# Optimization experiments

Hardware: AMD Instinct MI355X
Metric: run time of the kernel (lower is better)

Reference implementation:

```python
import jax, jax.numpy as jnp
import numpy as np

T = 0.07          # temperature (params[1])
B, N, D, C = 128, 100000, 128, 40  # batch, bank size (outputSize=K), feat dim (inputSize-1), n classes
STDV = 1.0 / np.sqrt((D + 1) / 3.0)  # init scale from __init__


def setup_inputs() -> dict:
    key = jax.random.key(0)
    k1, k2, k3, k4, k5, k6 = jax.random.split(key, 6)
    x = jax.random.normal(k1, (B, D), dtype=jnp.float32)
    x = x / jnp.linalg.norm(x, axis=1, keepdims=True)  # unit-norm features (keeps exp(out/T) in range)
    y = jax.random.randint(k2, (B,), 0, N)
    labels = jax.random.randint(k3, (B,), 0, C)
    bank_labels = jax.random.randint(k4, (N,), 0, C).astype(jnp.float32)
    mem_feats = (jax.random.uniform(k5, (N, D), dtype=jnp.float32) * 2.0 - 1.0) * STDV
    da_feats = (jax.random.uniform(k6, (N, D), dtype=jnp.float32) * 2.0 - 1.0) * STDV
    memory = jnp.concatenate([bank_labels[:, None], mem_feats], axis=1)      # [N, 1+D], col 0 = label
    memory_da = jnp.concatenate([bank_labels[:, None], da_feats], axis=1)    # [N, 1+D], col 0 = label
    return {"x": x, "y": y, "labels": labels, "memory_da": memory_da, "memory": memory}


def reference(x, y, labels, memory_da, memory):
    # NCEFunction.forward: out[b,n] = exp(x[b] . memory_da[n,1:] / T), Z-normalized per row (Z<0 branch)
    n_out = memory_da.shape[0]
    feats = memory_da[:, 1:]                               # [N, D] gathered features
    out = jnp.exp(jnp.einsum('bd,nd->bn', x, feats) / T)   # [B, N] (torch bmm over repeated bank)
    Z1 = out.mean(axis=1, keepdims=True) * n_out           # per-row Z estimate
    out = out / Z1
    # idx: per-label torch.where loop -> expressed densely as a boolean match matrix [B, N]
    idx_mask = memory_da[None, :, 0] == labels[:, None].astype(memory_da.dtype)
    return out, idx_mask
```

## Files before the change

kernel.cpp:

```cpp
#include <hip/hip_runtime.h>
#include <hip/hip_bf16.h>

#define NB 128
#define NMEM 100000
#define ND 128
constexpr float T_INV = 1.0f / 0.07f;

constexpr int LROW = ND + 8;
constexpr int TILE = 128;
constexpr int NTILES = (NMEM + TILE - 1) / TILE;
constexpr int ZSTRIDE = 16;
constexpr int C4FULL = TILE * 129 / 4;
constexpr int NITER = (C4FULL + 255) / 256;

typedef __attribute__((ext_vector_type(8))) __bf16 bf16x8;
typedef __attribute__((ext_vector_type(4))) float f32x4;
struct bf4 { __bf16 a, b, c, d; };

template<bool PASS2>
__global__ __launch_bounds__(256, 2) void nce_pass(
    const float* __restrict__ x,
    const int* __restrict__ labels,
    const float* __restrict__ mem_da,
    float* __restrict__ zbuf,
    float* __restrict__ out,
    float* __restrict__ maskout)
{
  __shared__ __bf16 xs[NB * LROW];
  __shared__ __bf16 fs[TILE * LROW];
  __shared__ float lbl_n[TILE];
  __shared__ float lbl_b[NB];
  __shared__ float rz[NB];
  __shared__ float zl[NB];

  const int tid = threadIdx.x;
  const int t = blockIdx.x;
  const int count4 = (t == NTILES - 1) ? (NMEM - t * TILE) * 129 / 4 : C4FULL;

  const float4* f4 = (const float4*)(mem_da + (size_t)t * (TILE * 129));
  float4 fv[NITER];
  #pragma unroll
  for (int i = 0; i < NITER; ++i) {
    int idx = tid + i * 256;
    fv[i] = f4[idx < count4 ? idx : 0];
  }
  const float4* x4 = (const float4*)x;
  float4 xv[16];
  #pragma unroll
  for (int i = 0; i < 16; ++i) xv[i] = x4[tid + i * 256];

  #pragma unroll
  for (int i = 0; i < 16; ++i) {
    int g4 = tid + i * 256;
    int row = g4 >> 5;
    int col = (g4 & 31) * 4;
    *(bf4*)&xs[row * LROW + col] =
        bf4{(__bf16)xv[i].x, (__bf16)xv[i].y, (__bf16)xv[i].z, (__bf16)xv[i].w};
  }

  #pragma unroll
  for (int i = 0; i < NITER; ++i) {
    int idx = tid + i * 256;
    if (idx < count4) {
      unsigned g = 4u * (unsigned)idx;
      unsigned r = g / 129u;
      unsigned cc = g - r * 129u;
      float4 v = fv[i];
      #pragma unroll
      for (int c = 0; c < 4; ++c) {
        float val = (&v.x)[c];
        if (cc == 0) lbl_n[r] = val;
        else fs[r * LROW + (cc - 1)] = (__bf16)val;
        if (++cc == 129u) { cc = 0; ++r; }
      }
    }
  }

  if (tid < NB) {
    lbl_b[tid] = (float)labels[tid];
    if (PASS2) rz[tid] = 1.0f / zbuf[tid * ZSTRIDE];
    else zl[tid] = 0.0f;
  }
  __syncthreads();

  const int wid = tid >> 6;
  const int lane = tid & 63;
  const int q = lane >> 4;
  const int l16 = lane & 15;
  const int nbase = t * TILE + wid * 32;

  if (nbase < NMEM) {
    f32x4 acc[8][2];
    #pragma unroll
    for (int mt = 0; mt < 8; ++mt) {
      acc[mt][0] = (f32x4){0.f, 0.f, 0.f, 0.f};
      acc[mt][1] = (f32x4){0.f, 0.f, 0.f, 0.f};
    }
    #pragma unroll
    for (int kc = 0; kc < 4; ++kc) {
      const int ko = kc * 32 + q * 8;
      bf16x8 b0 = *(const bf16x8*)&fs[(wid * 32 + l16) * LROW + ko];
      bf16x8 b1 = *(const bf16x8*)&fs[(wid * 32 + 16 + l16) * LROW + ko];
      #pragma unroll
      for (int mt = 0; mt < 8; ++mt) {
        bf16x8 a = *(const bf16x8*)&xs[(mt * 16 + l16) * LROW + ko];
        acc[mt][0] = __builtin_amdgcn_mfma_f32_16x16x32_bf16(a, b0, acc[mt][0], 0, 0, 0);
        acc[mt][1] = __builtin_amdgcn_mfma_f32_16x16x32_bf16(a, b1, acc[mt][1], 0, 0, 0);
      }
    }

    if (!PASS2) {
      float ln0 = lbl_n[wid * 32 + l16];
      float ln1 = lbl_n[wid * 32 + 16 + l16];
      #pragma unroll
      for (int mt = 0; mt < 8; ++mt) {
        #pragma unroll
        for (int r = 0; r < 4; ++r) {
          int m = mt * 16 + q * 4 + r;
          float lb = lbl_b[m];
          size_t base = (size_t)m * NMEM + nbase + l16;
          maskout[base]      = (ln0 == lb) ? 1.0f : 0.0f;
          maskout[base + 16] = (ln1 == lb) ? 1.0f : 0.0f;
          float v = __expf(acc[mt][0][r] * T_INV) + __expf(acc[mt][1][r] * T_INV);
          v += __shfl_xor(v, 1);
          v += __shfl_xor(v, 2);
          v += __shfl_xor(v, 4);
          v += __shfl_xor(v, 8);
          if (l16 == 0) atomicAdd(&zl[m], v);
        }
      }
    } else {
      #pragma unroll
      for (int mt = 0; mt < 8; ++mt) {
        #pragma unroll
        for (int r = 0; r < 4; ++r) {
          int m = mt * 16 + q * 4 + r;
          float rzm = rz[m];
          size_t base = (size_t)m * NMEM + nbase + l16;
          out[base]      = __expf(acc[mt][0][r] * T_INV) * rzm;
          out[base + 16] = __expf(acc[mt][1][r] * T_INV) * rzm;
        }
      }
    }
  }

  if (!PASS2) {
    __syncthreads();
    if (tid < NB) atomicAdd(&zbuf[tid * ZSTRIDE], zl[tid]);
  }
}

extern "C" void kernel_launch(void* const* d_in, const int* in_sizes, int n_in,
                              void* d_out, int out_size, void* d_ws, size_t ws_size,
                              hipStream_t stream) {
  const float* x      = (const float*)d_in[0];
  const int* labels   = (const int*)d_in[2];
  const float* mem_da = (const float*)d_in[3];
  float* out     = (float*)d_out;
  float* maskout = out + (size_t)NB * NMEM;
  float* zbuf    = (float*)d_ws;

  hipMemsetAsync(zbuf, 0, NB * ZSTRIDE * sizeof(float), stream);
  nce_pass<false><<<NTILES, 256, 0, stream>>>(x, labels, mem_da, zbuf, nullptr, maskout);
  nce_pass<true ><<<NTILES, 256, 0, stream>>>(x, labels, mem_da, zbuf, out, nullptr);
}
```

Before: 224.9 us.

## Convert both passes to persistent blocks with atomic tile queue and register prefetch

Replaces the one-block-per-tile launch with a fixed 512-block persistent grid that pulls tiles from a global atomic counter. While the current tile is computed, each block prefetches the next tile's memory bank rows into registers. This spreads the x staging and per-block setup over many tiles and overlaps global loads with MFMA and store work. The cost is an extra atomic and a barrier per tile, plus higher register pressure from holding the prefetch buffer alongside the accumulators.

```diff
diff --git a/kernel.cpp b/kernel.cpp
--- a/kernel.cpp
+++ b/kernel.cpp
@@ -8,10 +8,11 @@
 
 constexpr int LROW = ND + 8;
 constexpr int TILE = 128;
-constexpr int NTILES = (NMEM + TILE - 1) / TILE;
+constexpr int NT = (NMEM + TILE - 1) / TILE;
+constexpr int C4FULL = TILE * 129 / 4;
+constexpr int NIT = 17;
 constexpr int ZSTRIDE = 16;
-constexpr int C4FULL = TILE * 129 / 4;
-constexpr int NITER = (C4FULL + 255) / 256;
+constexpr int GRID = 512;
 
 typedef __attribute__((ext_vector_type(8))) __bf16 bf16x8;
 typedef __attribute__((ext_vector_type(4))) float f32x4;
@@ -23,6 +24,7 @@
     const int* __restrict__ labels,
     const float* __restrict__ mem_da,
     float* __restrict__ zbuf,
+    int* __restrict__ ctr,
     float* __restrict__ out,
     float* __restrict__ maskout)
 {
@@ -32,120 +34,129 @@
   __shared__ float lbl_b[NB];
   __shared__ float rz[NB];
   __shared__ float zl[NB];
+  __shared__ int cur;
 
   const int tid = threadIdx.x;
-  const int t = blockIdx.x;
-  const int count4 = (t == NTILES - 1) ? (NMEM - t * TILE) * 129 / 4 : C4FULL;
 
-  const float4* f4 = (const float4*)(mem_da + (size_t)t * (TILE * 129));
-  float4 fv[NITER];
-  #pragma unroll
-  for (int i = 0; i < NITER; ++i) {
-    int idx = tid + i * 256;
-    fv[i] = f4[idx < count4 ? idx : 0];
-  }
   const float4* x4 = (const float4*)x;
   float4 xv[16];
   #pragma unroll
   for (int i = 0; i < 16; ++i) xv[i] = x4[tid + i * 256];
-
   #pragma unroll
   for (int i = 0; i < 16; ++i) {
     int g4 = tid + i * 256;
-    int row = g4 >> 5;
-    int col = (g4 & 31) * 4;
-    *(bf4*)&xs[row * LROW + col] =
+    *(bf4*)&xs[(g4 >> 5) * LROW + (g4 & 31) * 4] =
         bf4{(__bf16)xv[i].x, (__bf16)xv[i].y, (__bf16)xv[i].z, (__bf16)xv[i].w};
   }
-
-  #pragma unroll
-  for (int i = 0; i < NITER; ++i) {
-    int idx = tid + i * 256;
-    if (idx < count4) {
-      unsigned g = 4u * (unsigned)idx;
-      unsigned r = g / 129u;
-      unsigned cc = g - r * 129u;
-      float4 v = fv[i];
-      #pragma unroll
-      for (int c = 0; c < 4; ++c) {
-        float val = (&v.x)[c];
-        if (cc == 0) lbl_n[r] = val;
-        else fs[r * LROW + (cc - 1)] = (__bf16)val;
-        if (++cc == 129u) { cc = 0; ++r; }
-      }
-    }
-  }
-
   if (tid < NB) {
     lbl_b[tid] = (float)labels[tid];
     if (PASS2) rz[tid] = 1.0f / zbuf[tid * ZSTRIDE];
-    else zl[tid] = 0.0f;
+    else zl[tid] = 0.f;
   }
+
+  if (tid == 0) cur = atomicAdd(ctr, 1);
   __syncthreads();
+  int t = cur;
 
-  const int wid = tid >> 6;
-  const int lane = tid & 63;
-  const int q = lane >> 4;
-  const int l16 = lane & 15;
-  const int nbase = t * TILE + wid * 32;
+  float4 fv[NIT];
+  auto prefetch = [&](int tt) {
+    const float4* f4 = (const float4*)(mem_da + (size_t)tt * (TILE * 129));
+    const int c4 = (tt == NT - 1) ? (NMEM - tt * TILE) * 129 / 4 : C4FULL;
+    #pragma unroll
+    for (int i = 0; i < NIT; ++i) {
+      int idx = tid + i * 256;
+      fv[i] = f4[idx < c4 ? idx : 0];
+    }
+  };
+  if (t < NT) prefetch(t);
 
-  if (nbase < NMEM) {
-    f32x4 acc[8][2];
+  const int wid = tid >> 6, lane = tid & 63, q = lane >> 4, l16 = lane & 15;
+
+  while (t < NT) {
+    const int rows = min(TILE, NMEM - t * TILE);
+    const int c4 = rows * 129 / 4;
     #pragma unroll
-    for (int mt = 0; mt < 8; ++mt) {
-      acc[mt][0] = (f32x4){0.f, 0.f, 0.f, 0.f};
-      acc[mt][1] = (f32x4){0.f, 0.f, 0.f, 0.f};
-    }
-    #pragma unroll
-    for (int kc = 0; kc < 4; ++kc) {
-      const int ko = kc * 32 + q * 8;
-      bf16x8 b0 = *(const bf16x8*)&fs[(wid * 32 + l16) * LROW + ko];
-      bf16x8 b1 = *(const bf16x8*)&fs[(wid * 32 + 16 + l16) * LROW + ko];
-      #pragma unroll
-      for (int mt = 0; mt < 8; ++mt) {
-        bf16x8 a = *(const bf16x8*)&xs[(mt * 16 + l16) * LROW + ko];
-        acc[mt][0] = __builtin_amdgcn_mfma_f32_16x16x32_bf16(a, b0, acc[mt][0], 0, 0, 0);
-        acc[mt][1] = __builtin_amdgcn_mfma_f32_16x16x32_bf16(a, b1, acc[mt][1], 0, 0, 0);
-      }
-    }
-
-    if (!PASS2) {
-      float ln0 = lbl_n[wid * 32 + l16];
-      float ln1 = lbl_n[wid * 32 + 16 + l16];
-      #pragma unroll
-      for (int mt = 0; mt < 8; ++mt) {
+    for (int i = 0; i < NIT; ++i) {
+      int idx = tid + i * 256;
+      if (idx < c4) {
+        unsigned g = 4u * (unsigned)idx;
+        unsigned r = g / 129u;
+        unsigned cc = g - r * 129u;
+        float4 v = fv[i];
         #pragma unroll
-        for (int r = 0; r < 4; ++r) {
-          int m = mt * 16 + q * 4 + r;
-          float lb = lbl_b[m];
-          size_t base = (size_t)m * NMEM + nbase + l16;
-          maskout[base]      = (ln0 == lb) ? 1.0f : 0.0f;
-          maskout[base + 16] = (ln1 == lb) ? 1.0f : 0.0f;
-          float v = __expf(acc[mt][0][r] * T_INV) + __expf(acc[mt][1][r] * T_INV);
-          v += __shfl_xor(v, 1);
-          v += __shfl_xor(v, 2);
-          v += __shfl_xor(v, 4);
-          v += __shfl_xor(v, 8);
-          if (l16 == 0) atomicAdd(&zl[m], v);
-        }
-      }
-    } else {
-      #pragma unroll
-      for (int mt = 0; mt < 8; ++mt) {
-        #pragma unroll
-        for (int r = 0; r < 4; ++r) {
-          int m = mt * 16 + q * 4 + r;
-          float rzm = rz[m];
-          size_t base = (size_t)m * NMEM + nbase + l16;
-          out[base]      = __expf(acc[mt][0][r] * T_INV) * rzm;
-          out[base + 16] = __expf(acc[mt][1][r] * T_INV) * rzm;
+        for (int c = 0; c < 4; ++c) {
+          float val = (&v.x)[c];
+          if (cc == 0) lbl_n[r] = val;
+          else fs[r * LROW + (cc - 1)] = (__bf16)val;
+          if (++cc == 129u) { cc = 0; ++r; }
         }
       }
     }
+    if (tid == 0) cur = atomicAdd(ctr, 1);
+    __syncthreads();
+    const int tn = cur;
+    if (tn < NT) prefetch(tn);
+
+    const int ntb = rows >> 5;
+    if (wid < ntb) {
+      f32x4 acc[8][2];
+      #pragma unroll
+      for (int mt = 0; mt < 8; ++mt) {
+        acc[mt][0] = (f32x4){0.f, 0.f, 0.f, 0.f};
+        acc[mt][1] = (f32x4){0.f, 0.f, 0.f, 0.f};
+      }
+      #pragma unroll
+      for (int kc = 0; kc < 4; ++kc) {
+        const int ko = kc * 32 + q * 8;
+        bf16x8 b0 = *(const bf16x8*)&fs[(wid * 32 + l16) * LROW + ko];
+        bf16x8 b1 = *(const bf16x8*)&fs[(wid * 32 + 16 + l16) * LROW + ko];
+        #pragma unroll
+        for (int mt = 0; mt < 8; ++mt) {
+          bf16x8 a = *(const bf16x8*)&xs[(mt * 16 + l16) * LROW + ko];
+          acc[mt][0] = __builtin_amdgcn_mfma_f32_16x16x32_bf16(a, b0, acc[mt][0], 0, 0, 0);
+          acc[mt][1] = __builtin_amdgcn_mfma_f32_16x16x32_bf16(a, b1, acc[mt][1], 0, 0, 0);
+        }
+      }
+      const size_t nb0 = (size_t)t * TILE + wid * 32 + l16;
+      if (!PASS2) {
+        float ln0 = lbl_n[wid * 32 + l16];
+        float ln1 = lbl_n[wid * 32 + 16 + l16];
+        #pragma unroll
+        for (int mt = 0; mt < 8; ++mt) {
+          #pragma unroll
+          for (int r = 0; r < 4; ++r) {
+            int m = mt * 16 + q * 4 + r;
+            float lb = lbl_b[m];
+            size_t base = (size_t)m * NMEM + nb0;
+            maskout[base]      = (ln0 == lb) ? 1.0f : 0.0f;
+            maskout[base + 16] = (ln1 == lb) ? 1.0f : 0.0f;
+            float v = __expf(acc[mt][0][r] * T_INV) + __expf(acc[mt][1][r] * T_INV);
+            v += __shfl_xor(v, 1);
+            v += __shfl_xor(v, 2);
+            v += __shfl_xor(v, 4);
+            v += __shfl_xor(v, 8);
+            if (l16 == 0) atomicAdd(&zl[m], v);
+          }
+        }
+      } else {
+        #pragma unroll
+        for (int mt = 0; mt < 8; ++mt) {
+          #pragma unroll
+          for (int r = 0; r < 4; ++r) {
+            int m = mt * 16 + q * 4 + r;
+            float rzm = rz[m];
+            size_t base = (size_t)m * NMEM + nb0;
+            out[base]      = __expf(acc[mt][0][r] * T_INV) * rzm;
+            out[base + 16] = __expf(acc[mt][1][r] * T_INV) * rzm;
+          }
+        }
+      }
+    }
+    __syncthreads();
+    t = tn;
   }
 
   if (!PASS2) {
-    __syncthreads();
     if (tid < NB) atomicAdd(&zbuf[tid * ZSTRIDE], zl[tid]);
   }
 }
@@ -159,8 +170,10 @@
   float* out     = (float*)d_out;
   float* maskout = out + (size_t)NB * NMEM;
   float* zbuf    = (float*)d_ws;
+  int* ctrA      = (int*)((char*)d_ws + 8192);
+  int* ctrB      = (int*)((char*)d_ws + 8192 + 64);
 
-  hipMemsetAsync(zbuf, 0, NB * ZSTRIDE * sizeof(float), stream);
-  nce_pass<false><<<NTILES, 256, 0, stream>>>(x, labels, mem_da, zbuf, nullptr, maskout);
-  nce_pass<true ><<<NTILES, 256, 0, stream>>>(x, labels, mem_da, zbuf, out, nullptr);
+  hipMemsetAsync(d_ws, 0, 8192 + 128, stream);
+  nce_pass<false><<<GRID, 256, 0, stream>>>(x, labels, mem_da, zbuf, ctrA, nullptr, maskout);
+  nce_pass<true ><<<GRID, 256, 0, stream>>>(x, labels, mem_da, zbuf, ctrB, out, nullptr);
 }
```

New measurement: 334.3 us. +48.6%, slower.
